# Optimization experiments

Measured on AMD Instinct MI355X. Metric: run time of the kernel, lower is better.

The kernel has to match this reference:

```python
import jax, jax.numpy as jnp
import numpy as np

N_WIRES = 4
N_LAYERS = 3
N_PPL = 8  # n_params_per_layer
N_PATCH = 196  # 14*14 2x2 patches of a 28x28 image


def _expand(t, ndim):
    # right-pad singleton dims so t broadcasts against an array of rank `ndim`
    return t.reshape(t.shape + (1,) * (ndim - t.ndim))


def apply_ry(state, theta, wire):
    # state: (B, P, 2,2,2,2) complex; wire axis = 2 + wire (wire 0 = MSB, torchquantum convention)
    s = jnp.moveaxis(state, 2 + wire, -1)
    a0, a1 = s[..., 0], s[..., 1]
    th = jnp.asarray(theta, dtype=jnp.float32)
    c = _expand(jnp.cos(th / 2), a0.ndim)
    sn = _expand(jnp.sin(th / 2), a0.ndim)
    s = jnp.stack([c * a0 - sn * a1, sn * a0 + c * a1], axis=-1)
    return jnp.moveaxis(s, -1, 2 + wire)


def apply_rz(state, theta, wire):
    s = jnp.moveaxis(state, 2 + wire, -1)
    th = jnp.asarray(theta, dtype=jnp.float32)
    ph = jnp.exp(-0.5j * th.astype(jnp.complex64))
    ph = _expand(ph, s.ndim - 1)
    s = jnp.stack([ph * s[..., 0], jnp.conj(ph) * s[..., 1]], axis=-1)
    return jnp.moveaxis(s, -1, 2 + wire)


def apply_cx(state, control, target):
    s = jnp.moveaxis(state, (2 + control, 2 + target), (-2, -1))
    s = jnp.concatenate([s[..., 0:1, :], s[..., 1:2, ::-1]], axis=-2)
    return jnp.moveaxis(s, (-2, -1), (2 + control, 2 + target))


def extract_patches(x):
    # x: (B,1,28,28) -> (B,196,4) with pixel order [(r,c),(r,c+1),(r+1,c),(r+1,c+1)]
    B = x.shape[0]
    x = x.reshape(B, 28, 28).reshape(B, 14, 2, 14, 2)
    x = jnp.transpose(x, (0, 1, 3, 2, 4))  # (B,14,14,2,2)
    return x.reshape(B, N_PATCH, 4)


def simulate(data, vparams):
    # data: (B,P,4) encoder angles; vparams: (n_layers, n_params_per_layer)
    B, P, _ = data.shape
    state = jnp.zeros((B, P, 16), dtype=jnp.complex64).at[..., 0].set(1.0)
    state = state.reshape(B, P, 2, 2, 2, 2)
    # encoder: RY(data[w]) on wire w (GeneralEncoder resets to |0..0> first)
    for w in range(N_WIRES):
        state = apply_ry(state, data[..., w], w)
    # variational layers (parameter-shared across patches/batch)
    for l in range(N_LAYERS):
        p = vparams[l]
        for i in range(N_WIRES):
            state = apply_ry(state, p[i % N_PPL], i)
            state = apply_rz(state, p[(i + 1) % N_PPL], i)
        for i in range(N_WIRES):
            state = apply_cx(state, i, (i + 1) % N_WIRES)
    # <Z_w> for each wire
    probs = state.real ** 2 + state.imag ** 2  # (B,P,2,2,2,2)
    exps = []
    for w in range(N_WIRES):
        other = tuple(2 + a for a in range(N_WIRES) if a != w)
        pw = probs.sum(axis=other)  # (B,P,2)
        exps.append(pw[..., 0] - pw[..., 1])
    return jnp.stack(exps, axis=-1)  # (B,P,4)


def setup_inputs() -> dict:
    key = jax.random.key(0)
    k1, k2, k3 = jax.random.split(key, 3)
    B = 4096
    x = jax.random.uniform(k1, (B, 1, 28, 28), dtype=jnp.float32)
    vparams = jax.random.normal(k2, (N_LAYERS, N_PPL), dtype=jnp.float32)
    W = jax.random.normal(k3, (10, 4 * 14 * 14), dtype=jnp.float32) * 0.03
    b = jnp.zeros((10,), dtype=jnp.float32)
    return {"x": x, "vparams": vparams, "W": W, "b": b}


def reference(x, vparams, W, b):
    B = x.shape[0]
    data = extract_patches(x)                     # (B,196,4)
    feats = simulate(data, vparams).reshape(B, -1)  # (B,784), patch-major like torch.cat
    logits = feats @ W.T + b                      # (B,10)
    return jax.nn.log_softmax(logits, axis=-1)
```

## Files before the change

### kernel.cpp

```cpp
#include <hip/hip_runtime.h>
#include <hip/hip_bf16.h>


#define NPATCH 196

__global__ void qc_build_C(const float* __restrict__ vp,
                           float* __restrict__ Cout) {
  __shared__ float Ur[16][16];
  __shared__ float Ui[16][16];
  __shared__ float M[4][16][16];
  int t = threadIdx.x;

  if (t < 16) {
    float sr[16], si[16];
#pragma unroll
    for (int i = 0; i < 16; ++i) { sr[i] = 0.f; si[i] = 0.f; }
    sr[t] = 1.f;

    for (int l = 0; l < 3; ++l) {
#pragma unroll
      for (int w = 0; w < 4; ++w) {
        float thy = vp[l * 8 + (w % 8)];
        float thz = vp[l * 8 + ((w + 1) % 8)];
        float cy, sy, cz, sz;
        __sincosf(0.5f * thy, &sy, &cy);
        __sincosf(0.5f * thz, &sz, &cz);
        const int bit = 8 >> w;
#pragma unroll
        for (int i = 0; i < 16; ++i) {
          if (!(i & bit)) {
            int i1 = i | bit;
            float a0r = sr[i], a0i = si[i], a1r = sr[i1], a1i = si[i1];
            sr[i]  = cy * a0r - sy * a1r;  si[i]  = cy * a0i - sy * a1i;
            sr[i1] = sy * a0r + cy * a1r;  si[i1] = sy * a0i + cy * a1i;
          }
        }
#pragma unroll
        for (int i = 0; i < 16; ++i) {
          float r = sr[i], m = si[i];
          if (i & bit) { sr[i] = r * cz - m * sz; si[i] = m * cz + r * sz; }
          else         { sr[i] = r * cz + m * sz; si[i] = m * cz - r * sz; }
        }
      }
#pragma unroll
      for (int w = 0; w < 4; ++w) {
        const int cbit = 8 >> w;
        const int tbit = 8 >> ((w + 1) & 3);
#pragma unroll
        for (int i = 0; i < 16; ++i) {
          if ((i & cbit) && !(i & tbit)) {
            int i1 = i | tbit;
            float tr = sr[i], ti = si[i];
            sr[i] = sr[i1]; si[i] = si[i1];
            sr[i1] = tr;    si[i1] = ti;
          }
        }
      }
    }
#pragma unroll
    for (int i = 0; i < 16; ++i) { Ur[i][t] = sr[i]; Ui[i][t] = si[i]; }
  }
  __syncthreads();

  for (int e = t; e < 1024; e += 64) {
    int w = e >> 8, r = (e >> 4) & 15, c = e & 15;
    float acc = 0.f;
#pragma unroll
    for (int i = 0; i < 16; ++i) {
      float sgn = ((i >> (3 - w)) & 1) ? -1.f : 1.f;
      acc += sgn * (Ur[i][r] * Ur[i][c] + Ui[i][r] * Ui[i][c]);
    }
    M[w][r][c] = acc;
  }
  __syncthreads();

  const int pj1[10] = {0, 0, 0, 0, 1, 1, 1, 2, 2, 3};
  const int pj2[10] = {0, 1, 2, 3, 1, 2, 3, 2, 3, 3};
  for (int e = t; e < 400; e += 64) {
    int w = e / 100;
    int rem = e - w * 100;
    int a = rem / 10;
    int bq = rem - a * 10;
    int j1 = pj1[a], j2 = pj2[a], k1 = pj1[bq], k2 = pj2[bq];
    float v = M[w][4 * j1 + k1][4 * j2 + k2];
    if (k1 != k2) v += M[w][4 * j1 + k2][4 * j2 + k1];
    if (j1 != j2) {
      v += M[w][4 * j2 + k1][4 * j1 + k2];
      if (k1 != k2) v += M[w][4 * j2 + k2][4 * j1 + k1];
    }
    Cout[e] = v;
  }
}

__global__ __launch_bounds__(256) void qc_fused(const float* __restrict__ x,
                                                const float* __restrict__ C,
                                                const float4* __restrict__ W4,
                                                const float* __restrict__ bias,
                                                float* __restrict__ out) {
  int b = blockIdx.x;
  int p = threadIdx.x;

  float lg[10];
#pragma unroll
  for (int c = 0; c < 10; ++c) lg[c] = 0.f;

  if (p < NPATCH) {
    int pr = p / 14;
    int pc = p - pr * 14;
    const float* xb = x + (size_t)b * 784;
    float2 top = *(const float2*)(xb + (2 * pr) * 28 + 2 * pc);
    float2 bot = *(const float2*)(xb + (2 * pr + 1) * 28 + 2 * pc);
    float s0, c0, s1, c1, s2, c2, s3, c3;
    __sincosf(0.5f * top.x, &s0, &c0);
    __sincosf(0.5f * top.y, &s1, &c1);
    __sincosf(0.5f * bot.x, &s2, &c2);
    __sincosf(0.5f * bot.y, &s3, &c3);

    float p0 = c0 * c1, p1 = c0 * s1, p2 = s0 * c1, p3 = s0 * s1;
    float q0 = c2 * c3, q1 = c2 * s3, q2 = s2 * c3, q3 = s2 * s3;

    float P[10] = {p0 * p0, p0 * p1, p0 * p2, p0 * p3, p1 * p1,
                   p1 * p2, p1 * p3, p2 * p2, p2 * p3, p3 * p3};
    float Q[10] = {q0 * q0, q0 * q1, q0 * q2, q0 * q3, q1 * q1,
                   q1 * q2, q1 * q3, q2 * q2, q2 * q3, q3 * q3};

    float e[4];
#pragma unroll
    for (int w = 0; w < 4; ++w) {
      float acc = 0.f;
#pragma unroll
      for (int a = 0; a < 10; ++a) {
        const float* row = C + (w * 10 + a) * 10;
        float tt = row[0] * Q[0] + row[1] * Q[1] + row[2] * Q[2] +
                   row[3] * Q[3] + row[4] * Q[4] + row[5] * Q[5] +
                   row[6] * Q[6] + row[7] * Q[7] + row[8] * Q[8] +
                   row[9] * Q[9];
        acc += P[a] * tt;
      }
      e[w] = acc;
    }

    float4 f = make_float4(e[0], e[1], e[2], e[3]);
#pragma unroll
    for (int c = 0; c < 10; ++c) {
      float4 w = W4[c * NPATCH + p];
      lg[c] = f.x * w.x + f.y * w.y + f.z * w.z + f.w * w.w;
    }
  }

#pragma unroll
  for (int off = 32; off >= 1; off >>= 1)
#pragma unroll
    for (int c = 0; c < 10; ++c)
      lg[c] += __shfl_xor(lg[c], off, 64);

  __shared__ float red[4][10];
  int wave = threadIdx.x >> 6;
  int lane = threadIdx.x & 63;
  if (lane == 0) {
#pragma unroll
    for (int c = 0; c < 10; ++c) red[wave][c] = lg[c];
  }
  __syncthreads();

  if (threadIdx.x == 0) {
    float L[10], m = -1e30f;
#pragma unroll
    for (int c = 0; c < 10; ++c) {
      L[c] = red[0][c] + red[1][c] + red[2][c] + red[3][c] + bias[c];
      m = fmaxf(m, L[c]);
    }
    float ssum = 0.f;
#pragma unroll
    for (int c = 0; c < 10; ++c) ssum += __expf(L[c] - m);
    float ls = m + __logf(ssum);
#pragma unroll
    for (int c = 0; c < 10; ++c) out[b * 10 + c] = L[c] - ls;
  }
}

extern "C" void kernel_launch(void* const* d_in, const int* in_sizes, int n_in,
                              void* d_out, int out_size, void* d_ws, size_t ws_size,
                              hipStream_t stream) {
  const float* x    = (const float*)d_in[0];
  const float* vp   = (const float*)d_in[1];
  const float* W    = (const float*)d_in[2];
  const float* bias = (const float*)d_in[3];
  float* out = (float*)d_out;

  int B = in_sizes[0] / 784;

  float* Cws = (float*)d_ws;

  qc_build_C<<<1, 64, 0, stream>>>(vp, Cws);

  qc_fused<<<B, 256, 0, stream>>>(x, Cws, (const float4*)W, bias, out);
}
```

Before: 102.9 us.

## Fuse circuit-coefficient build into main kernel, recomputing per block in shared memory

Merges the single-block kernel that builds the 400-entry quadratic-form coefficient table into the per-sample kernel. Every block now recomputes the 16x16 circuit unitary, the Z-observable matrices and the coefficient table in shared memory, padded to float4 rows for vectorized LDS reads. This removes one kernel launch and the serial dependency between the two kernels. In exchange each of the 4096 blocks repeats the unitary simulation on only 16 threads, with extra barriers, before its main work starts.

```diff
diff --git a/kernel.cpp b/kernel.cpp
--- a/kernel.cpp
+++ b/kernel.cpp
@@ -4,12 +4,19 @@
 
 #define NPATCH 196
 
-__global__ void qc_build_C(const float* __restrict__ vp,
-                           float* __restrict__ Cout) {
+__global__ __launch_bounds__(256) void qc_all(const float* __restrict__ x,
+                                              const float* __restrict__ vp,
+                                              const float4* __restrict__ W4,
+                                              const float* __restrict__ bias,
+                                              float* __restrict__ out) {
   __shared__ float Ur[16][16];
   __shared__ float Ui[16][16];
   __shared__ float M[4][16][16];
-  int t = threadIdx.x;
+  __shared__ float4 sC[160];
+  __shared__ float red[4][10];
+
+  const int t = threadIdx.x;
+  const int b = blockIdx.x;
 
   if (t < 16) {
     float sr[16], si[16];
@@ -62,7 +69,8 @@
   }
   __syncthreads();
 
-  for (int e = t; e < 1024; e += 64) {
+#pragma unroll
+  for (int e = t; e < 1024; e += 256) {
     int w = e >> 8, r = (e >> 4) & 15, c = e & 15;
     float acc = 0.f;
 #pragma unroll
@@ -74,42 +82,41 @@
   }
   __syncthreads();
 
-  const int pj1[10] = {0, 0, 0, 0, 1, 1, 1, 2, 2, 3};
-  const int pj2[10] = {0, 1, 2, 3, 1, 2, 3, 2, 3, 3};
-  for (int e = t; e < 400; e += 64) {
-    int w = e / 100;
-    int rem = e - w * 100;
-    int a = rem / 10;
-    int bq = rem - a * 10;
-    int j1 = pj1[a], j2 = pj2[a], k1 = pj1[bq], k2 = pj2[bq];
-    float v = M[w][4 * j1 + k1][4 * j2 + k2];
-    if (k1 != k2) v += M[w][4 * j1 + k2][4 * j2 + k1];
-    if (j1 != j2) {
-      v += M[w][4 * j2 + k1][4 * j1 + k2];
-      if (k1 != k2) v += M[w][4 * j2 + k2][4 * j1 + k1];
-    }
-    Cout[e] = v;
-  }
-}
-
-__global__ __launch_bounds__(256) void qc_fused(const float* __restrict__ x,
-                                                const float* __restrict__ C,
-                                                const float4* __restrict__ W4,
-                                                const float* __restrict__ bias,
-                                                float* __restrict__ out) {
-  int b = blockIdx.x;
-  int p = threadIdx.x;
+  {
+    const int pj1[10] = {0, 0, 0, 0, 1, 1, 1, 2, 2, 3};
+    const int pj2[10] = {0, 1, 2, 3, 1, 2, 3, 2, 3, 3};
+    float* sCf = (float*)sC;
+    for (int e = t; e < 640; e += 256) {
+      int row = e >> 4;
+      int col = e & 15;
+      float v = 0.f;
+      if (col < 10) {
+        int w = row / 10;
+        int a = row - w * 10;
+        int j1 = pj1[a], j2 = pj2[a], k1 = pj1[col], k2 = pj2[col];
+        v = M[w][4 * j1 + k1][4 * j2 + k2];
+        if (k1 != k2) v += M[w][4 * j1 + k2][4 * j2 + k1];
+        if (j1 != j2) {
+          v += M[w][4 * j2 + k1][4 * j1 + k2];
+          if (k1 != k2) v += M[w][4 * j2 + k2][4 * j1 + k1];
+        }
+      }
+      sCf[e] = v;
+    }
+  }
+  __syncthreads();
 
   float lg[10];
 #pragma unroll
   for (int c = 0; c < 10; ++c) lg[c] = 0.f;
 
-  if (p < NPATCH) {
-    int pr = p / 14;
-    int pc = p - pr * 14;
+  if (t < NPATCH) {
+    int pr = t / 14;
+    int pc = t - pr * 14;
     const float* xb = x + (size_t)b * 784;
-    float2 top = *(const float2*)(xb + (2 * pr) * 28 + 2 * pc);
-    float2 bot = *(const float2*)(xb + (2 * pr + 1) * 28 + 2 * pc);
+    float2 top = *(const float2*)(xb + 56 * pr + 2 * pc);
+    float2 bot = *(const float2*)(xb + 56 * pr + 28 + 2 * pc);
+
     float s0, c0, s1, c1, s2, c2, s3, c3;
     __sincosf(0.5f * top.x, &s0, &c0);
     __sincosf(0.5f * top.y, &s1, &c1);
@@ -130,11 +137,13 @@
       float acc = 0.f;
 #pragma unroll
       for (int a = 0; a < 10; ++a) {
-        const float* row = C + (w * 10 + a) * 10;
-        float tt = row[0] * Q[0] + row[1] * Q[1] + row[2] * Q[2] +
-                   row[3] * Q[3] + row[4] * Q[4] + row[5] * Q[5] +
-                   row[6] * Q[6] + row[7] * Q[7] + row[8] * Q[8] +
-                   row[9] * Q[9];
+        int base = (w * 10 + a) * 4;
+        float4 r0 = sC[base];
+        float4 r1 = sC[base + 1];
+        float4 r2 = sC[base + 2];
+        float tt = r0.x * Q[0] + r0.y * Q[1] + r0.z * Q[2] + r0.w * Q[3]
+                 + r1.x * Q[4] + r1.y * Q[5] + r1.z * Q[6] + r1.w * Q[7]
+                 + r2.x * Q[8] + r2.y * Q[9];
         acc += P[a] * tt;
       }
       e[w] = acc;
@@ -143,7 +152,7 @@
     float4 f = make_float4(e[0], e[1], e[2], e[3]);
 #pragma unroll
     for (int c = 0; c < 10; ++c) {
-      float4 w = W4[c * NPATCH + p];
+      float4 w = W4[c * NPATCH + t];
       lg[c] = f.x * w.x + f.y * w.y + f.z * w.z + f.w * w.w;
     }
   }
@@ -154,16 +163,15 @@
     for (int c = 0; c < 10; ++c)
       lg[c] += __shfl_xor(lg[c], off, 64);
 
-  __shared__ float red[4][10];
-  int wave = threadIdx.x >> 6;
-  int lane = threadIdx.x & 63;
+  int wave = t >> 6;
+  int lane = t & 63;
   if (lane == 0) {
 #pragma unroll
     for (int c = 0; c < 10; ++c) red[wave][c] = lg[c];
   }
   __syncthreads();
 
-  if (threadIdx.x == 0) {
+  if (t == 0) {
     float L[10], m = -1e30f;
 #pragma unroll
     for (int c = 0; c < 10; ++c) {
@@ -190,9 +198,5 @@
 
   int B = in_sizes[0] / 784;
 
-  float* Cws = (float*)d_ws;
-
-  qc_build_C<<<1, 64, 0, stream>>>(vp, Cws);
-
-  qc_fused<<<B, 256, 0, stream>>>(x, Cws, (const float4*)W, bias, out);
+  qc_all<<<B, 256, 0, stream>>>(x, vp, (const float4*)W, bias, out);
 }
```

After: 121.1 us. 1.18x slower.
